# Performance work log

Measured on AMD Instinct MI355X. Metric: run time of the kernel, lower is better.

The kernel has to match this reference:

```python
import jax, jax.numpy as jnp
import numpy as np

SIGMA_MIN = 0.01
LOG_2PI = float(np.log(2.0 * np.pi))


def setup_inputs() -> dict:
    key = jax.random.key(0)
    ks = jax.random.split(key, 7)
    B, S, K = 256, 2048, 20
    return {
        "xs": jax.random.normal(ks[0], (B, S, 5), dtype=jnp.float32),
        "logits_pred": jax.random.normal(ks[1], (B, S, K), dtype=jnp.float32),
        "mus_pred": jax.random.normal(ks[2], (B, S, K, 2), dtype=jnp.float32),
        "sigmas_x": jax.random.uniform(ks[3], (B, S, K), dtype=jnp.float32),
        "sigmas_y": jax.random.uniform(ks[4], (B, S, K), dtype=jnp.float32),
        "sigmas_xy": jax.random.normal(ks[5], (B, S, K), dtype=jnp.float32),
        "pen_pred": jax.random.normal(ks[6], (B, S, 3), dtype=jnp.float32),
    }


def _losses(xs, logits_pred, mus_pred, sigmas_x, sigmas_y, sigmas_xy, pen_pred):
    positions_true = xs[:, :, :2]          # [B,S,2]
    pen_true = xs[:, :, 2:]                # [B,S,3]

    # relative positions: roll(-1) along seq then diff
    positions_next = jnp.roll(positions_true, -1, axis=1)
    rel = positions_next - positions_true  # [B,S,2]

    # Cholesky factor entries (L = [[sx,0],[sxy,sy]]), clamped as in torch
    sx = jnp.maximum(sigmas_x, SIGMA_MIN)                        # [B,S,K]
    sy = jnp.maximum(sigmas_y, SIGMA_MIN)
    sxy = jnp.clip(sigmas_xy, -SIGMA_MIN, SIGMA_MIN)

    # closed-form 2x2 MVN log_prob via triangular solve
    d1 = rel[:, :, None, 0] - mus_pred[..., 0]                   # [B,S,K]
    d2 = rel[:, :, None, 1] - mus_pred[..., 1]
    z1 = d1 / sx
    z2 = (d2 - sxy * z1) / sy
    comp_logp = -0.5 * (z1 * z1 + z2 * z2) - LOG_2PI - jnp.log(sx) - jnp.log(sy)

    # mixture log-prob: logsumexp over components with normalized mixing logits
    log_mix = jax.nn.log_softmax(logits_pred, axis=-1)           # [B,S,K]
    logp = jax.nn.logsumexp(log_mix + comp_logp, axis=-1)        # [B,S]
    position_loss = -jnp.mean(logp)

    # pen cross-entropy with soft (probability) targets, mean over B*S
    log_probs = jax.nn.log_softmax(pen_pred, axis=-1)            # [B,S,3]
    pen_loss = -jnp.mean(jnp.sum(pen_true * log_probs, axis=-1))
    return position_loss, pen_loss


def reference(xs, logits_pred, mus_pred, sigmas_x, sigmas_y, sigmas_xy, pen_pred):
    return _losses(xs, logits_pred, mus_pred, sigmas_x, sigmas_y, sigmas_xy, pen_pred)
```

## Files before the change

kernel.cpp:

```cpp
#include <hip/hip_runtime.h>
#include <math.h>

static constexpr int S_LEN = 2048;
static constexpr int KMIX  = 20;
static constexpr int NROWS = 256 * 2048;
static constexpr int BLOCK = 256;
static constexpr int NBLK  = NROWS / BLOCK;
static constexpr float SIGMA_MIN_F = 0.01f;
static constexpr float LOG_2PI_F   = 1.8378770664093453f;

__global__ __launch_bounds__(BLOCK) void sketch_loss_kernel(
    const float* __restrict__ xs,
    const float* __restrict__ logits,
    const float* __restrict__ mus,
    const float* __restrict__ sxp,
    const float* __restrict__ syp,
    const float* __restrict__ sxyp,
    const float* __restrict__ pen,
    float* __restrict__ partials)
{
    const int r = blockIdx.x * BLOCK + threadIdx.x;

    const float4* lg4  = (const float4*)(logits + (size_t)r * KMIX);
    const float4* sx4  = (const float4*)(sxp    + (size_t)r * KMIX);
    const float4* sy4  = (const float4*)(syp    + (size_t)r * KMIX);
    const float4* sxy4 = (const float4*)(sxyp   + (size_t)r * KMIX);
    const float4* mu4  = (const float4*)(mus    + (size_t)r * KMIX * 2);

    float4 L[5], X[5], Y[5], W[5], MA[5], MB[5];
    #pragma unroll
    for (int c = 0; c < 5; ++c) L[c] = lg4[c];
    #pragma unroll
    for (int c = 0; c < 5; ++c) X[c] = sx4[c];
    #pragma unroll
    for (int c = 0; c < 5; ++c) Y[c] = sy4[c];
    #pragma unroll
    for (int c = 0; c < 5; ++c) W[c] = sxy4[c];
    #pragma unroll
    for (int c = 0; c < 5; ++c) { MA[c] = mu4[2 * c]; MB[c] = mu4[2 * c + 1]; }

    const int s = r & (S_LEN - 1);
    const float* xr = xs + (size_t)r * 5;
    const float x0 = xr[0], x1 = xr[1];
    const float pt0 = xr[2], pt1 = xr[3], pt2 = xr[4];
    const int rn = (s == S_LEN - 1) ? (r - (S_LEN - 1)) : (r + 1);
    const float* xnr = xs + (size_t)rn * 5;
    const float xn0 = xnr[0], xn1 = xnr[1];

    const float* pr = pen + (size_t)r * 3;
    const float q0 = pr[0], q1 = pr[1], q2 = pr[2];

    __builtin_amdgcn_sched_barrier(0);

    const float rel0 = xn0 - x0;
    const float rel1 = xn1 - x1;

    float m_a = -INFINITY, s_a = 0.0f;
    float m_l = -INFINITY, s_l = 0.0f;

    #pragma unroll
    for (int c = 0; c < 5; ++c) {
        const float lv[4]  = {L[c].x, L[c].y, L[c].z, L[c].w};
        const float sxa[4] = {X[c].x, X[c].y, X[c].z, X[c].w};
        const float sya[4] = {Y[c].x, Y[c].y, Y[c].z, Y[c].w};
        const float swa[4] = {W[c].x, W[c].y, W[c].z, W[c].w};
        const float mu_[8] = {MA[c].x, MA[c].y, MA[c].z, MA[c].w,
                              MB[c].x, MB[c].y, MB[c].z, MB[c].w};

        float av[4];
        #pragma unroll
        for (int j = 0; j < 4; ++j) {
            const float sx  = fmaxf(sxa[j], SIGMA_MIN_F);
            const float sy  = fmaxf(sya[j], SIGMA_MIN_F);
            const float sxy = fminf(fmaxf(swa[j], -SIGMA_MIN_F), SIGMA_MIN_F);
            const float d1 = rel0 - mu_[2 * j];
            const float d2 = rel1 - mu_[2 * j + 1];
            const float z1 = d1 / sx;
            const float z2 = (d2 - sxy * z1) / sy;
            av[j] = lv[j] - 0.5f * (z1 * z1 + z2 * z2) - LOG_2PI_F - __logf(sx * sy);
        }

        const float cma = fmaxf(fmaxf(av[0], av[1]), fmaxf(av[2], av[3]));
        if (cma > m_a) { s_a *= __expf(m_a - cma); m_a = cma; }
        s_a += __expf(av[0] - m_a) + __expf(av[1] - m_a)
             + __expf(av[2] - m_a) + __expf(av[3] - m_a);

        const float cml = fmaxf(fmaxf(lv[0], lv[1]), fmaxf(lv[2], lv[3]));
        if (cml > m_l) { s_l *= __expf(m_l - cml); m_l = cml; }
        s_l += __expf(lv[0] - m_l) + __expf(lv[1] - m_l)
             + __expf(lv[2] - m_l) + __expf(lv[3] - m_l);
    }

    float acc_pos = (m_a + __logf(s_a)) - (m_l + __logf(s_l));

    const float mq = fmaxf(fmaxf(q0, q1), q2);
    const float lseq = mq + __logf(__expf(q0 - mq) + __expf(q1 - mq) + __expf(q2 - mq));
    float acc_pen = pt0 * (q0 - lseq) + pt1 * (q1 - lseq) + pt2 * (q2 - lseq);

    const int lane = threadIdx.x & 63;
    const int wid  = threadIdx.x >> 6;
    #pragma unroll
    for (int off = 32; off > 0; off >>= 1) {
        acc_pos += __shfl_down(acc_pos, off, 64);
        acc_pen += __shfl_down(acc_pen, off, 64);
    }
    __shared__ float s_pos[4], s_pen[4];
    if (lane == 0) { s_pos[wid] = acc_pos; s_pen[wid] = acc_pen; }
    __syncthreads();
    if (threadIdx.x == 0) {
        partials[blockIdx.x * 2 + 0] = s_pos[0] + s_pos[1] + s_pos[2] + s_pos[3];
        partials[blockIdx.x * 2 + 1] = s_pen[0] + s_pen[1] + s_pen[2] + s_pen[3];
    }
}

__global__ __launch_bounds__(BLOCK) void sketch_reduce_kernel(
    const float* __restrict__ partials, float* __restrict__ out)
{
    float tp = 0.0f, te = 0.0f;
    for (int i = threadIdx.x; i < NBLK; i += BLOCK) {
        tp += partials[2 * i + 0];
        te += partials[2 * i + 1];
    }
    #pragma unroll
    for (int off = 32; off > 0; off >>= 1) {
        tp += __shfl_down(tp, off, 64);
        te += __shfl_down(te, off, 64);
    }
    __shared__ float sp[4], se[4];
    const int lane = threadIdx.x & 63;
    const int wid  = threadIdx.x >> 6;
    if (lane == 0) { sp[wid] = tp; se[wid] = te; }
    __syncthreads();
    if (threadIdx.x == 0) {
        const float P = sp[0] + sp[1] + sp[2] + sp[3];
        const float E = se[0] + se[1] + se[2] + se[3];
        out[0] = -P / (float)NROWS;
        out[1] = -E / (float)NROWS;
    }
}

extern "C" void kernel_launch(void* const* d_in, const int* in_sizes, int n_in,
                              void* d_out, int out_size, void* d_ws, size_t ws_size,
                              hipStream_t stream) {
    const float* xs     = (const float*)d_in[0];
    const float* logits = (const float*)d_in[1];
    const float* mus    = (const float*)d_in[2];
    const float* sx     = (const float*)d_in[3];
    const float* sy     = (const float*)d_in[4];
    const float* sxy    = (const float*)d_in[5];
    const float* pen    = (const float*)d_in[6];
    float* out = (float*)d_out;
    float* partials = (float*)d_ws;

    sketch_loss_kernel<<<NBLK, BLOCK, 0, stream>>>(xs, logits, mus, sx, sy, sxy, pen, partials);
    sketch_reduce_kernel<<<1, BLOCK, 0, stream>>>(partials, out);
}
```

Measured before the change: 48.37 us.

## Split each row across two threads and fold log terms into reciprocal weights

Each row's 20 mixture components are now handled by two threads (10 each), with max and sum combined through xor shuffles, which doubles thread count and shortens per-thread load chains. The per-component log(sx*sy) is replaced by multiplying the exponentials by a reciprocal 1/(sx*sy), with a fixed offset added to the max so the result stays in range. Divisions become one hardware reciprocal per component. The aim is more memory-level parallelism and fewer transcendental operations, at the cost of extra shuffles, redundant per-row xs/pen loads, and a fixed-offset stabilisation that could lose precision for extreme sigma values.

```diff
diff --git a/kernel.cpp b/kernel.cpp
--- a/kernel.cpp
+++ b/kernel.cpp
@@ -5,9 +5,11 @@
 static constexpr int KMIX  = 20;
 static constexpr int NROWS = 256 * 2048;
 static constexpr int BLOCK = 256;
-static constexpr int NBLK  = NROWS / BLOCK;
+static constexpr int ROWS_PER_BLOCK = BLOCK / 2;
+static constexpr int NBLK  = NROWS / ROWS_PER_BLOCK;
 static constexpr float SIGMA_MIN_F = 0.01f;
 static constexpr float LOG_2PI_F   = 1.8378770664093453f;
+static constexpr float TMAX_LOG_F  = 9.2103403719761836f;
 
 __global__ __launch_bounds__(BLOCK) void sketch_loss_kernel(
     const float* __restrict__ xs,
@@ -19,30 +21,33 @@
     const float* __restrict__ pen,
     float* __restrict__ partials)
 {
-    const int r = blockIdx.x * BLOCK + threadIdx.x;
+    const int tid = blockIdx.x * BLOCK + threadIdx.x;
+    const int r   = tid >> 1;
+    const int h   = tid & 1;
 
-    const float4* lg4  = (const float4*)(logits + (size_t)r * KMIX);
-    const float4* sx4  = (const float4*)(sxp    + (size_t)r * KMIX);
-    const float4* sy4  = (const float4*)(syp    + (size_t)r * KMIX);
-    const float4* sxy4 = (const float4*)(sxyp   + (size_t)r * KMIX);
-    const float4* mu4  = (const float4*)(mus    + (size_t)r * KMIX * 2);
+    const float2* lg2  = (const float2*)(logits + (size_t)r * KMIX + h * 10);
+    const float2* sx2  = (const float2*)(sxp    + (size_t)r * KMIX + h * 10);
+    const float2* sy2  = (const float2*)(syp    + (size_t)r * KMIX + h * 10);
+    const float2* sw2  = (const float2*)(sxyp   + (size_t)r * KMIX + h * 10);
+    const float4* mu4  = (const float4*)(mus    + (size_t)r * (2 * KMIX) + h * 20);
 
-    float4 L[5], X[5], Y[5], W[5], MA[5], MB[5];
+    float2 L[5], X[5], Y[5], W[5];
+    float4 M[5];
     #pragma unroll
-    for (int c = 0; c < 5; ++c) L[c] = lg4[c];
+    for (int c = 0; c < 5; ++c) L[c] = lg2[c];
     #pragma unroll
-    for (int c = 0; c < 5; ++c) X[c] = sx4[c];
+    for (int c = 0; c < 5; ++c) X[c] = sx2[c];
     #pragma unroll
-    for (int c = 0; c < 5; ++c) Y[c] = sy4[c];
+    for (int c = 0; c < 5; ++c) Y[c] = sy2[c];
     #pragma unroll
-    for (int c = 0; c < 5; ++c) W[c] = sxy4[c];
+    for (int c = 0; c < 5; ++c) W[c] = sw2[c];
     #pragma unroll
-    for (int c = 0; c < 5; ++c) { MA[c] = mu4[2 * c]; MB[c] = mu4[2 * c + 1]; }
+    for (int c = 0; c < 5; ++c) M[c] = mu4[c];
 
-    const int s = r & (S_LEN - 1);
     const float* xr = xs + (size_t)r * 5;
     const float x0 = xr[0], x1 = xr[1];
     const float pt0 = xr[2], pt1 = xr[3], pt2 = xr[4];
+    const int s = r & (S_LEN - 1);
     const int rn = (s == S_LEN - 1) ? (r - (S_LEN - 1)) : (r + 1);
     const float* xnr = xs + (size_t)rn * 5;
     const float xn0 = xnr[0], xn1 = xnr[1];
@@ -55,57 +60,63 @@
     const float rel0 = xn0 - x0;
     const float rel1 = xn1 - x1;
 
-    float m_a = -INFINITY, s_a = 0.0f;
-    float m_l = -INFINITY, s_l = 0.0f;
+    float u[10], t[10], lv[10];
+    #pragma unroll
+    for (int c = 0; c < 10; ++c) {
+        const float l_  = (c & 1) ? L[c >> 1].y : L[c >> 1].x;
+        const float sxv = (c & 1) ? X[c >> 1].y : X[c >> 1].x;
+        const float syv = (c & 1) ? Y[c >> 1].y : Y[c >> 1].x;
+        const float swv = (c & 1) ? W[c >> 1].y : W[c >> 1].x;
+        const float m0  = (c & 1) ? M[c >> 1].z : M[c >> 1].x;
+        const float m1  = (c & 1) ? M[c >> 1].w : M[c >> 1].y;
 
-    #pragma unroll
-    for (int c = 0; c < 5; ++c) {
-        const float lv[4]  = {L[c].x, L[c].y, L[c].z, L[c].w};
-        const float sxa[4] = {X[c].x, X[c].y, X[c].z, X[c].w};
-        const float sya[4] = {Y[c].x, Y[c].y, Y[c].z, Y[c].w};
-        const float swa[4] = {W[c].x, W[c].y, W[c].z, W[c].w};
-        const float mu_[8] = {MA[c].x, MA[c].y, MA[c].z, MA[c].w,
-                              MB[c].x, MB[c].y, MB[c].z, MB[c].w};
-
-        float av[4];
-        #pragma unroll
-        for (int j = 0; j < 4; ++j) {
-            const float sx  = fmaxf(sxa[j], SIGMA_MIN_F);
-            const float sy  = fmaxf(sya[j], SIGMA_MIN_F);
-            const float sxy = fminf(fmaxf(swa[j], -SIGMA_MIN_F), SIGMA_MIN_F);
-            const float d1 = rel0 - mu_[2 * j];
-            const float d2 = rel1 - mu_[2 * j + 1];
-            const float z1 = d1 / sx;
-            const float z2 = (d2 - sxy * z1) / sy;
-            av[j] = lv[j] - 0.5f * (z1 * z1 + z2 * z2) - LOG_2PI_F - __logf(sx * sy);
-        }
-
-        const float cma = fmaxf(fmaxf(av[0], av[1]), fmaxf(av[2], av[3]));
-        if (cma > m_a) { s_a *= __expf(m_a - cma); m_a = cma; }
-        s_a += __expf(av[0] - m_a) + __expf(av[1] - m_a)
-             + __expf(av[2] - m_a) + __expf(av[3] - m_a);
-
-        const float cml = fmaxf(fmaxf(lv[0], lv[1]), fmaxf(lv[2], lv[3]));
-        if (cml > m_l) { s_l *= __expf(m_l - cml); m_l = cml; }
-        s_l += __expf(lv[0] - m_l) + __expf(lv[1] - m_l)
-             + __expf(lv[2] - m_l) + __expf(lv[3] - m_l);
+        const float sx = fmaxf(sxv, SIGMA_MIN_F);
+        const float sy = fmaxf(syv, SIGMA_MIN_F);
+        const float sw = fminf(fmaxf(swv, -SIGMA_MIN_F), SIGMA_MIN_F);
+        const float tc = __builtin_amdgcn_rcpf(sx * sy);
+        const float d1 = rel0 - m0;
+        const float d2 = rel1 - m1;
+        const float z1 = d1 * sy * tc;
+        const float z2 = (d2 - sw * z1) * sx * tc;
+        lv[c] = l_;
+        t[c]  = tc;
+        u[c]  = l_ - 0.5f * (z1 * z1 + z2 * z2) - LOG_2PI_F;
     }
 
-    float acc_pos = (m_a + __logf(s_a)) - (m_l + __logf(s_l));
+    float mu_ = u[0], ml_ = lv[0];
+    #pragma unroll
+    for (int c = 1; c < 10; ++c) { mu_ = fmaxf(mu_, u[c]); ml_ = fmaxf(ml_, lv[c]); }
+    mu_ = fmaxf(mu_, __shfl_xor(mu_, 1, 64));
+    ml_ = fmaxf(ml_, __shfl_xor(ml_, 1, 64));
+    const float mhat = mu_ + TMAX_LOG_F;
+
+    float s1 = 0.0f, s2 = 0.0f;
+    #pragma unroll
+    for (int c = 0; c < 10; ++c) {
+        s1 += t[c] * __expf(u[c] - mhat);
+        s2 += __expf(lv[c] - ml_);
+    }
+    s1 += __shfl_xor(s1, 1, 64);
+    s2 += __shfl_xor(s2, 1, 64);
+
+    const float logp = (mhat + __logf(s1)) - (ml_ + __logf(s2));
 
     const float mq = fmaxf(fmaxf(q0, q1), q2);
     const float lseq = mq + __logf(__expf(q0 - mq) + __expf(q1 - mq) + __expf(q2 - mq));
-    float acc_pen = pt0 * (q0 - lseq) + pt1 * (q1 - lseq) + pt2 * (q2 - lseq);
+    const float penv = pt0 * (q0 - lseq) + pt1 * (q1 - lseq) + pt2 * (q2 - lseq);
+
+    float accp = logp * 0.5f;
+    float acce = penv * 0.5f;
 
     const int lane = threadIdx.x & 63;
     const int wid  = threadIdx.x >> 6;
     #pragma unroll
     for (int off = 32; off > 0; off >>= 1) {
-        acc_pos += __shfl_down(acc_pos, off, 64);
-        acc_pen += __shfl_down(acc_pen, off, 64);
+        accp += __shfl_down(accp, off, 64);
+        acce += __shfl_down(acce, off, 64);
     }
     __shared__ float s_pos[4], s_pen[4];
-    if (lane == 0) { s_pos[wid] = acc_pos; s_pen[wid] = acc_pen; }
+    if (lane == 0) { s_pos[wid] = accp; s_pen[wid] = acce; }
     __syncthreads();
     if (threadIdx.x == 0) {
         partials[blockIdx.x * 2 + 0] = s_pos[0] + s_pos[1] + s_pos[2] + s_pos[3];
@@ -113,11 +124,11 @@
     }
 }
 
-__global__ __launch_bounds__(BLOCK) void sketch_reduce_kernel(
+__global__ __launch_bounds__(256) void sketch_reduce_kernel(
     const float* __restrict__ partials, float* __restrict__ out)
 {
     float tp = 0.0f, te = 0.0f;
-    for (int i = threadIdx.x; i < NBLK; i += BLOCK) {
+    for (int i = threadIdx.x; i < NBLK; i += 256) {
         tp += partials[2 * i + 0];
         te += partials[2 * i + 1];
     }
@@ -153,5 +164,5 @@
     float* partials = (float*)d_ws;
 
     sketch_loss_kernel<<<NBLK, BLOCK, 0, stream>>>(xs, logits, mus, sx, sy, sxy, pen, partials);
-    sketch_reduce_kernel<<<1, BLOCK, 0, stream>>>(partials, out);
+    sketch_reduce_kernel<<<1, 256, 0, stream>>>(partials, out);
 }
```

Result: no change. 48.30 us (-0.2%).
